# Kernel tuning notes

Hardware: AMD Instinct MI355X
Metric: run time of the kernel (lower is better)

Reference implementation:

```python
import jax, jax.numpy as jnp
import numpy as np

K_DIM = 768
HEADS = 8
HEAD_DIM = K_DIM // HEADS  # 96


def setup_inputs() -> dict:
    key = jax.random.key(0)
    ks = jax.random.split(key, 6)
    b, t = 4, 2048
    scale = 1.0 / np.sqrt(HEAD_DIM)
    return {
        "input_x": jax.random.normal(ks[0], (b, t, K_DIM), dtype=jnp.float32),
        "Wq": jax.random.normal(ks[1], (HEAD_DIM, HEAD_DIM), dtype=jnp.float32) * scale,
        "Wk": jax.random.normal(ks[2], (HEAD_DIM, HEAD_DIM), dtype=jnp.float32) * scale,
        "Wv": jax.random.normal(ks[3], (HEAD_DIM, HEAD_DIM), dtype=jnp.float32) * scale,
        "Wu": jax.random.normal(ks[4], (K_DIM, K_DIM), dtype=jnp.float32) * (1.0 / np.sqrt(K_DIM)),
        "bu": jax.random.normal(ks[5], (K_DIM,), dtype=jnp.float32) * 0.01,
    }


def reference(input_x, Wq, Wk, Wv, Wu, bu):
    b, t, k = input_x.shape
    h, d = HEADS, k // HEADS
    # split into heads: [b, t, h, d]; per-head projections share the same d x d weights
    x = input_x.reshape(b, t, h, d)
    inv4 = 1.0 / (k ** 0.25)
    q = jnp.einsum("bthd,od->btho", x, Wq) * inv4  # scaled queries
    kk = jnp.einsum("bthd,od->btho", x, Wk) * inv4  # scaled keys
    v = jnp.einsum("bthd,od->btho", x, Wv)
    # full attention matrix [b, h, t, t] (materialized, as in the original bmm impl)
    scores = jnp.einsum("bthd,bshd->bhts", q, kk)
    attn = jax.nn.softmax(scores, axis=-1)
    out = jnp.einsum("bhts,bshd->bthd", attn, v).reshape(b, t, k)
    return out @ Wu.T + bu
```

## Files before the change

kernel.cpp:

```cpp
#include <hip/hip_runtime.h>
#include <hip/hip_bf16.h>
#include <math.h>

#define TB 2048
#define NB 4
#define NH 8
#define HD 96
#define KD 768

typedef unsigned short u16;
typedef __attribute__((ext_vector_type(4))) u16 u16x4;
typedef __attribute__((ext_vector_type(8))) u16 u16x8;
typedef __attribute__((ext_vector_type(4))) float f32x4;
typedef __attribute__((ext_vector_type(16))) float f32x16;
typedef __attribute__((ext_vector_type(4))) unsigned u32x4;
typedef __attribute__((ext_vector_type(8))) __bf16 bf16x8;

__device__ __forceinline__ u16 f2bf(float f) {
    unsigned u = __builtin_bit_cast(unsigned, f);
    u += 0x7FFFu + ((u >> 16) & 1u);
    return (u16)(u >> 16);
}
__device__ __forceinline__ bf16x8 cast8(u16x8 u) { return __builtin_bit_cast(bf16x8, u); }
__device__ __forceinline__ unsigned pkbf(float a, float b) {
    unsigned w;
    asm("v_cvt_pk_bf16_f32 %0, %1, %2" : "=v"(w) : "v"(a), "v"(b));
    return w;
}

__global__ __launch_bounds__(256) void qkv_proj(
    const float* __restrict__ x, const float* __restrict__ Wq,
    const float* __restrict__ Wk, const float* __restrict__ Wv,
    u16* __restrict__ Q, u16* __restrict__ Kout, u16* __restrict__ VT, float inv4)
{
    __shared__ __align__(16) u16 Wl[3][96][104];
    const int tid = threadIdx.x;
    for (int idx = tid; idx < 3 * 9216; idx += 256) {
        int m = idx / 9216, rem = idx % 9216;
        const float* Wsrc = (m == 0) ? Wq : (m == 1) ? Wk : Wv;
        float scale = (m < 2) ? inv4 : 1.0f;
        int r = rem / 96, c = rem % 96;
        Wl[m][r][c] = f2bf(Wsrc[rem] * scale);
    }
    __syncthreads();

    const int w = tid >> 6, l = tid & 63;
    const int lc = l & 15, lk = l >> 4;
    const int bh = blockIdx.y, b = bh >> 3, h = bh & 7;
    const int t0 = blockIdx.x * 64 + w * 16;

    bf16x8 afrag[3];
    {
        const float* xp = x + ((long)((b * TB + t0 + lc) * NH + h)) * HD + 8 * lk;
#pragma unroll
        for (int c = 0; c < 3; ++c) {
            f32x4 f0 = *(const f32x4*)(xp + c * 32);
            f32x4 f1 = *(const f32x4*)(xp + c * 32 + 4);
            u16x8 u;
#pragma unroll
            for (int j = 0; j < 4; ++j) { u[j] = f2bf(f0[j]); u[4 + j] = f2bf(f1[j]); }
            afrag[c] = cast8(u);
        }
    }

    const f32x4 Z4 = {0.f, 0.f, 0.f, 0.f};
    u16* outs[2] = {Q, Kout};
#pragma unroll
    for (int m = 0; m < 2; ++m) {
        f32x4 acc[6];
#pragma unroll
        for (int nt = 0; nt < 6; ++nt) acc[nt] = Z4;
#pragma unroll
        for (int c = 0; c < 3; ++c) {
#pragma unroll
            for (int nt = 0; nt < 6; ++nt) {
                u16x8 bw = *(const u16x8*)&Wl[m][nt * 16 + lc][c * 32 + 8 * lk];
                acc[nt] = __builtin_amdgcn_mfma_f32_16x16x32_bf16(afrag[c], cast8(bw), acc[nt], 0, 0, 0);
            }
        }
#pragma unroll
        for (int reg = 0; reg < 4; ++reg) {
            int t = t0 + lk * 4 + reg;
            u16* op = outs[m] + ((long)bh * TB + t) * HD;
#pragma unroll
            for (int nt = 0; nt < 6; ++nt)
                op[nt * 16 + lc] = f2bf(acc[nt][reg]);
        }
    }
    {
        f32x4 acc[6];
#pragma unroll
        for (int nt = 0; nt < 6; ++nt) acc[nt] = Z4;
#pragma unroll
        for (int c = 0; c < 3; ++c) {
#pragma unroll
            for (int nt = 0; nt < 6; ++nt) {
                u16x8 aw = *(const u16x8*)&Wl[2][nt * 16 + lc][c * 32 + 8 * lk];
                acc[nt] = __builtin_amdgcn_mfma_f32_16x16x32_bf16(cast8(aw), afrag[c], acc[nt], 0, 0, 0);
            }
        }
#pragma unroll
        for (int nt = 0; nt < 6; ++nt)
#pragma unroll
            for (int reg = 0; reg < 4; ++reg) {
                int o = nt * 16 + lk * 4 + reg;
                VT[((long)bh * HD + o) * TB + t0 + lc] = f2bf(acc[nt][reg]);
            }
    }
}

#define KOFF 0
#define VOFF (64 * 104)
#define SLAB (64 * 104 + 96 * 72)

__global__ __launch_bounds__(256) void attn(
    const u16* __restrict__ Q, const u16* __restrict__ Kin, const u16* __restrict__ VT,
    u16* __restrict__ O)
{
    __shared__ __align__(16) u16 SM[2][SLAB];

    const int tid = threadIdx.x;
    const int w = tid >> 6, l = tid & 63;
    const int m32 = l & 31, hi = l >> 5;
    const int lid = (blockIdx.x & 7) * 64 + (blockIdx.x >> 3);
    const int qt = lid & 15, bh = lid >> 4;
    const int q0 = qt * 128 + w * 32;

    const u16* Qb = Q + (long)bh * TB * HD;
    const u16* Kb = Kin + (long)bh * TB * HD;
    const u16* Vb = VT + (long)bh * HD * TB;

    const u16* gbase[6]; int loff[6]; int mult[6];
#pragma unroll
    for (int ci = 0; ci < 6; ++ci) {
        int ch = tid + ci * 256;
        if (ch < 768) {
            int row = ch / 12, cc = (ch % 12) * 8;
            gbase[ci] = Kb + row * HD + cc;
            mult[ci] = HD;
            loff[ci] = KOFF + row * 104 + cc;
        } else {
            int c2 = ch - 768;
            int d = c2 >> 3, sc = (c2 & 7) * 8;
            gbase[ci] = Vb + (long)d * TB + sc;
            mult[ci] = 1;
            loff[ci] = VOFF + d * 72 + sc;
        }
    }

    bf16x8 qb[6];
#pragma unroll
    for (int kk = 0; kk < 6; ++kk)
        qb[kk] = cast8(*(const u16x8*)(Qb + (long)(q0 + m32) * HD + kk * 16 + 8 * hi));

    u16x8 r[6];
#pragma unroll
    for (int ci = 0; ci < 6; ++ci) r[ci] = *(const u16x8*)(gbase[ci]);
#pragma unroll
    for (int ci = 0; ci < 6; ++ci) *(u16x8*)(SM[0] + loff[ci]) = r[ci];
#pragma unroll
    for (int ci = 0; ci < 6; ++ci) r[ci] = *(const u16x8*)(gbase[ci] + (long)64 * mult[ci]);

    float m_st = -1e30f, l_st = 0.f;
    f32x16 accO[3];
#pragma unroll
    for (int dt = 0; dt < 3; ++dt)
#pragma unroll
        for (int rr = 0; rr < 16; ++rr) accO[dt][rr] = 0.f;

    for (int st = 0; st < TB / 64; ++st) {
        __syncthreads();
        if (st < TB / 64 - 1) {
            u16* dst = SM[(st + 1) & 1];
#pragma unroll
            for (int ci = 0; ci < 6; ++ci) *(u16x8*)(dst + loff[ci]) = r[ci];
            int s2 = (st + 2 < TB / 64 ? st + 2 : TB / 64 - 1) * 64;
#pragma unroll
            for (int ci = 0; ci < 6; ++ci) r[ci] = *(const u16x8*)(gbase[ci] + (long)s2 * mult[ci]);
        }
        const u16* KP = SM[st & 1] + KOFF;
        const u16* VP = SM[st & 1] + VOFF;

        f32x16 sa[2];
        __builtin_amdgcn_s_setprio(1);
#pragma unroll
        for (int st2 = 0; st2 < 2; ++st2) {
#pragma unroll
            for (int rr = 0; rr < 16; ++rr) sa[st2][rr] = 0.f;
#pragma unroll
            for (int kk = 0; kk < 6; ++kk) {
                u16x8 kf = *(const u16x8*)(KP + (st2 * 32 + m32) * 104 + kk * 16 + 8 * hi);
                sa[st2] = __builtin_amdgcn_mfma_f32_32x32x16_bf16(cast8(kf), qb[kk], sa[st2], 0, 0, 0);
            }
        }
        __builtin_amdgcn_s_setprio(0);

        float tm = sa[0][0];
#pragma unroll
        for (int st2 = 0; st2 < 2; ++st2)
#pragma unroll
            for (int rr = 0; rr < 16; ++rr) tm = fmaxf(tm, sa[st2][rr]);
        tm = fmaxf(tm, __shfl_xor(tm, 32));
        if (!__all(tm - m_st <= 8.0f)) {
            float mnew = fmaxf(m_st, tm);
            float alpha = __expf(m_st - mnew);
#pragma unroll
            for (int dt = 0; dt < 3; ++dt)
#pragma unroll
                for (int rr = 0; rr < 16; ++rr) accO[dt][rr] *= alpha;
            l_st *= alpha;
            m_st = mnew;
        }
        float sum = 0.f;
#pragma unroll
        for (int st2 = 0; st2 < 2; ++st2)
#pragma unroll
            for (int rr = 0; rr < 16; ++rr) {
                float pv = __expf(sa[st2][rr] - m_st);
                sa[st2][rr] = pv;
                sum += pv;
            }
        sum += __shfl_xor(sum, 32);
        l_st += sum;

#pragma unroll
        for (int st2 = 0; st2 < 2; ++st2) {
            unsigned A1 = pkbf(sa[st2][0], sa[st2][1]);
            unsigned A2 = pkbf(sa[st2][2], sa[st2][3]);
            unsigned B1 = pkbf(sa[st2][4], sa[st2][5]);
            unsigned B2 = pkbf(sa[st2][6], sa[st2][7]);
            unsigned A3 = pkbf(sa[st2][8], sa[st2][9]);
            unsigned A4 = pkbf(sa[st2][10], sa[st2][11]);
            unsigned B3 = pkbf(sa[st2][12], sa[st2][13]);
            unsigned B4 = pkbf(sa[st2][14], sa[st2][15]);
            unsigned xA1 = __shfl_xor((int)A1, 32), xA2 = __shfl_xor((int)A2, 32);
            unsigned xB1 = __shfl_xor((int)B1, 32), xB2 = __shfl_xor((int)B2, 32);
            unsigned xA3 = __shfl_xor((int)A3, 32), xA4 = __shfl_xor((int)A4, 32);
            unsigned xB3 = __shfl_xor((int)B3, 32), xB4 = __shfl_xor((int)B4, 32);
            u32x4 t0 = { hi ? xB1 : A1, hi ? xB2 : A2, hi ? B1 : xA1, hi ? B2 : xA2 };
            u32x4 t1 = { hi ? xB3 : A3, hi ? xB4 : A4, hi ? B3 : xA3, hi ? B4 : xA4 };
            bf16x8 pb0 = __builtin_bit_cast(bf16x8, t0);
            bf16x8 pb1 = __builtin_bit_cast(bf16x8, t1);
            __builtin_amdgcn_s_setprio(1);
#pragma unroll
            for (int dt = 0; dt < 3; ++dt) {
                u16x8 vfa = *(const u16x8*)(VP + (dt * 32 + m32) * 72 + st2 * 32 + 8 * hi);
                accO[dt] = __builtin_amdgcn_mfma_f32_32x32x16_bf16(cast8(vfa), pb0, accO[dt], 0, 0, 0);
            }
#pragma unroll
            for (int dt = 0; dt < 3; ++dt) {
                u16x8 vfb = *(const u16x8*)(VP + (dt * 32 + m32) * 72 + st2 * 32 + 16 + 8 * hi);
                accO[dt] = __builtin_amdgcn_mfma_f32_32x32x16_bf16(cast8(vfb), pb1, accO[dt], 0, 0, 0);
            }
            __builtin_amdgcn_s_setprio(0);
        }
    }

    const int b = bh >> 3, h = bh & 7;
    float linv = 1.0f / l_st;
    int t = q0 + m32;
    u16* op = O + ((long)(b * TB + t)) * KD + h * HD;
#pragma unroll
    for (int dt = 0; dt < 3; ++dt)
#pragma unroll
        for (int q4 = 0; q4 < 4; ++q4) {
            u16x4 v = { f2bf(accO[dt][q4 * 4 + 0] * linv), f2bf(accO[dt][q4 * 4 + 1] * linv),
                        f2bf(accO[dt][q4 * 4 + 2] * linv), f2bf(accO[dt][q4 * 4 + 3] * linv) };
            *(u16x4*)(op + dt * 32 + q4 * 8 + 4 * hi) = v;
        }
}

__global__ __launch_bounds__(256) void wu_conv(const float* __restrict__ Wu, u16* __restrict__ Wub) {
    int i = (blockIdx.x * 256 + threadIdx.x) * 4;
    f32x4 f = *(const f32x4*)(Wu + i);
    u16x4 o = { f2bf(f[0]), f2bf(f[1]), f2bf(f[2]), f2bf(f[3]) };
    *(u16x4*)(Wub + i) = o;
}

__global__ __launch_bounds__(256) void out_gemm(
    const u16* __restrict__ O, const u16* __restrict__ Wub,
    const float* __restrict__ bu, float* __restrict__ out)
{
    __shared__ __align__(16) u16 Al[2][128][68];
    __shared__ __align__(16) u16 Bl[2][128][68];
    const int tid = threadIdx.x;
    const int w = tid >> 6, l = tid & 63;
    const int m32 = l & 31, hi = l >> 5;
    const int wr = w >> 1, wc = w & 1;
    const int lid = (blockIdx.x & 7) * 48 + (blockIdx.x >> 3);
    const int nb = lid % 6, mb = lid / 6;
    const int m0 = mb * 128, n0 = nb * 128;

    const int crow = tid >> 3, ccol = (tid & 7) * 8;

    f32x16 acc[2][2];
#pragma unroll
    for (int i = 0; i < 2; ++i)
#pragma unroll
        for (int j = 0; j < 2; ++j)
#pragma unroll
            for (int rr = 0; rr < 16; ++rr) acc[i][j][rr] = 0.f;

    u16x8 ra[4], rb[4];
#pragma unroll
    for (int i = 0; i < 4; ++i) {
        ra[i] = *(const u16x8*)(O   + (long)(m0 + crow + i * 32) * KD + ccol);
        rb[i] = *(const u16x8*)(Wub + (long)(n0 + crow + i * 32) * KD + ccol);
    }
#pragma unroll
    for (int i = 0; i < 4; ++i) {
        *(u16x8*)&Al[0][crow + i * 32][ccol] = ra[i];
        *(u16x8*)&Bl[0][crow + i * 32][ccol] = rb[i];
    }
#pragma unroll
    for (int i = 0; i < 4; ++i) {
        ra[i] = *(const u16x8*)(O   + (long)(m0 + crow + i * 32) * KD + 64 + ccol);
        rb[i] = *(const u16x8*)(Wub + (long)(n0 + crow + i * 32) * KD + 64 + ccol);
    }

    for (int kt = 0; kt < KD / 64; ++kt) {
        __syncthreads();
        if (kt < KD / 64 - 1) {
            int p = (kt + 1) & 1;
#pragma unroll
            for (int i = 0; i < 4; ++i) {
                *(u16x8*)&Al[p][crow + i * 32][ccol] = ra[i];
                *(u16x8*)&Bl[p][crow + i * 32][ccol] = rb[i];
            }
            int cn = (kt + 2 < KD / 64 ? kt + 2 : KD / 64 - 1) * 64;
#pragma unroll
            for (int i = 0; i < 4; ++i) {
                ra[i] = *(const u16x8*)(O   + (long)(m0 + crow + i * 32) * KD + cn + ccol);
                rb[i] = *(const u16x8*)(Wub + (long)(n0 + crow + i * 32) * KD + cn + ccol);
            }
        }
        int p = kt & 1;
        __builtin_amdgcn_s_setprio(1);
#pragma unroll
        for (int k16 = 0; k16 < 4; ++k16) {
            bf16x8 afr[2], bfr[2];
#pragma unroll
            for (int rb2 = 0; rb2 < 2; ++rb2)
                afr[rb2] = cast8(*(const u16x8*)&Al[p][wr * 64 + rb2 * 32 + m32][k16 * 16 + 8 * hi]);
#pragma unroll
            for (int cb2 = 0; cb2 < 2; ++cb2)
                bfr[cb2] = cast8(*(const u16x8*)&Bl[p][wc * 64 + cb2 * 32 + m32][k16 * 16 + 8 * hi]);
#pragma unroll
            for (int rb2 = 0; rb2 < 2; ++rb2)
#pragma unroll
                for (int cb2 = 0; cb2 < 2; ++cb2)
                    acc[rb2][cb2] = __builtin_amdgcn_mfma_f32_32x32x16_bf16(afr[rb2], bfr[cb2], acc[rb2][cb2], 0, 0, 0);
        }
        __builtin_amdgcn_s_setprio(0);
    }

    const float bv0 = bu[n0 + wc * 64 + m32];
    const float bv1 = bu[n0 + wc * 64 + 32 + m32];
#pragma unroll
    for (int rb2 = 0; rb2 < 2; ++rb2)
#pragma unroll
        for (int cb2 = 0; cb2 < 2; ++cb2) {
            float bv = cb2 ? bv1 : bv0;
            int nn = n0 + wc * 64 + cb2 * 32 + m32;
#pragma unroll
            for (int reg = 0; reg < 16; ++reg) {
                int mm = m0 + wr * 64 + rb2 * 32 + (reg & 3) + 8 * (reg >> 2) + 4 * hi;
                out[(long)mm * KD + nn] = acc[rb2][cb2][reg] + bv;
            }
        }
}

extern "C" void kernel_launch(void* const* d_in, const int* in_sizes, int n_in,
                              void* d_out, int out_size, void* d_ws, size_t ws_size,
                              hipStream_t stream) {
    const float* x  = (const float*)d_in[0];
    const float* Wq = (const float*)d_in[1];
    const float* Wk = (const float*)d_in[2];
    const float* Wv = (const float*)d_in[3];
    const float* Wu = (const float*)d_in[4];
    const float* bu = (const float*)d_in[5];
    float* out = (float*)d_out;

    u16* ws = (u16*)d_ws;
    const size_t SZ = (size_t)NB * NH * TB * HD;
    u16* Q   = ws;
    u16* Kq  = ws + SZ;
    u16* VT  = ws + 2 * SZ;
    u16* O   = ws + 3 * SZ;
    u16* Wub = ws;

    const float inv4 = 1.0f / powf((float)KD, 0.25f);

    qkv_proj<<<dim3(TB / 64, NB * NH), dim3(256), 0, stream>>>(x, Wq, Wk, Wv, Q, Kq, VT, inv4);
    attn<<<dim3(TB / 128 * NB * NH), dim3(256), 0, stream>>>(Q, Kq, VT, O);
    wu_conv<<<dim3((KD * KD) / 1024), dim3(256), 0, stream>>>(Wu, Wub);
    out_gemm<<<dim3((NB * TB / 128) * (KD / 128)), dim3(256), 0, stream>>>(O, Wub, bu, out);
}
```

Baseline: 208.8 us.

## Double query rows per wave in attention and stage QKV stores through LDS

The attention kernel now gives each wave 64 query rows (two 32-row sub-tiles) instead of 32, so each K/V fragment read from LDS feeds two MFMAs. The KV tile shrinks to 32 keys and the grid is halved, which cuts K/V global and LDS traffic per query. In exchange it raises register pressure from the doubled accumulators and leaves only 256 blocks. The QKV projection also stages its outputs in shared memory so Q/K/VT are written with coalesced 16-byte stores instead of scattered 2-byte stores, at the cost of extra barriers.

```diff
diff --git a/kernel.cpp b/kernel.cpp
--- a/kernel.cpp
+++ b/kernel.cpp
@@ -34,6 +34,7 @@
     u16* __restrict__ Q, u16* __restrict__ Kout, u16* __restrict__ VT, float inv4)
 {
     __shared__ __align__(16) u16 Wl[3][96][104];
+    __shared__ __align__(16) u16 Rp[96 * 72];
     const int tid = threadIdx.x;
     for (int idx = tid; idx < 3 * 9216; idx += 256) {
         int m = idx / 9216, rem = idx % 9216;
@@ -47,11 +48,12 @@
     const int w = tid >> 6, l = tid & 63;
     const int lc = l & 15, lk = l >> 4;
     const int bh = blockIdx.y, b = bh >> 3, h = bh & 7;
-    const int t0 = blockIdx.x * 64 + w * 16;
+    const int t0 = blockIdx.x * 64;
+    const int tw = t0 + w * 16;
 
     bf16x8 afrag[3];
     {
-        const float* xp = x + ((long)((b * TB + t0 + lc) * NH + h)) * HD + 8 * lk;
+        const float* xp = x + ((long)((b * TB + tw + lc) * NH + h)) * HD + 8 * lk;
 #pragma unroll
         for (int c = 0; c < 3; ++c) {
             f32x4 f0 = *(const f32x4*)(xp + c * 32);
@@ -78,13 +80,18 @@
                 acc[nt] = __builtin_amdgcn_mfma_f32_16x16x32_bf16(afrag[c], cast8(bw), acc[nt], 0, 0, 0);
             }
         }
-#pragma unroll
-        for (int reg = 0; reg < 4; ++reg) {
-            int t = t0 + lk * 4 + reg;
-            u16* op = outs[m] + ((long)bh * TB + t) * HD;
-#pragma unroll
-            for (int nt = 0; nt < 6; ++nt)
-                op[nt * 16 + lc] = f2bf(acc[nt][reg]);
+        __syncthreads();
+#pragma unroll
+        for (int nt = 0; nt < 6; ++nt)
+#pragma unroll
+            for (int reg = 0; reg < 4; ++reg)
+                Rp[(w * 16 + lk * 4 + reg) * 104 + nt * 16 + lc] = f2bf(acc[nt][reg]);
+        __syncthreads();
+#pragma unroll
+        for (int ci = 0; ci < 3; ++ci) {
+            int ch = tid + ci * 256;
+            int row = ch / 12, cc = (ch % 12) * 8;
+            *(u16x8*)(outs[m] + ((long)bh * TB + t0 + row) * HD + cc) = *(const u16x8*)&Rp[row * 104 + cc];
         }
     }
     {
@@ -99,175 +106,199 @@
                 acc[nt] = __builtin_amdgcn_mfma_f32_16x16x32_bf16(cast8(aw), afrag[c], acc[nt], 0, 0, 0);
             }
         }
+        __syncthreads();
 #pragma unroll
         for (int nt = 0; nt < 6; ++nt)
 #pragma unroll
             for (int reg = 0; reg < 4; ++reg) {
                 int o = nt * 16 + lk * 4 + reg;
-                VT[((long)bh * HD + o) * TB + t0 + lc] = f2bf(acc[nt][reg]);
-            }
-    }
-}
-
-#define KOFF 0
-#define VOFF (64 * 104)
-#define SLAB (64 * 104 + 96 * 72)
+                Rp[o * 72 + w * 16 + lc] = f2bf(acc[nt][reg]);
+            }
+        __syncthreads();
+#pragma unroll
+        for (int ci = 0; ci < 3; ++ci) {
+            int ch = tid + ci * 256;
+            int row = ch >> 3, tc = (ch & 7) * 8;
+            *(u16x8*)(VT + ((long)bh * HD + row) * TB + t0 + tc) = *(const u16x8*)&Rp[row * 72 + tc];
+        }
+    }
+}
+
+#define KVB 32
+#define VOFF2 (KVB * 104)
+#define SLAB2 (KVB * 104 + 96 * 40)
 
 __global__ __launch_bounds__(256) void attn(
     const u16* __restrict__ Q, const u16* __restrict__ Kin, const u16* __restrict__ VT,
     u16* __restrict__ O)
 {
-    __shared__ __align__(16) u16 SM[2][SLAB];
+    __shared__ __align__(16) u16 SM[2][SLAB2];
 
     const int tid = threadIdx.x;
     const int w = tid >> 6, l = tid & 63;
     const int m32 = l & 31, hi = l >> 5;
-    const int lid = (blockIdx.x & 7) * 64 + (blockIdx.x >> 3);
-    const int qt = lid & 15, bh = lid >> 4;
-    const int q0 = qt * 128 + w * 32;
+    const int lid = (blockIdx.x & 7) * 32 + (blockIdx.x >> 3);
+    const int qt = lid & 7, bh = lid >> 3;
+    const int q0 = qt * 256 + w * 64;
 
     const u16* Qb = Q + (long)bh * TB * HD;
     const u16* Kb = Kin + (long)bh * TB * HD;
     const u16* Vb = VT + (long)bh * HD * TB;
 
-    const u16* gbase[6]; int loff[6]; int mult[6];
-#pragma unroll
-    for (int ci = 0; ci < 6; ++ci) {
+    const u16* gbase[3]; int loff[3]; int mult[3];
+#pragma unroll
+    for (int ci = 0; ci < 3; ++ci) {
         int ch = tid + ci * 256;
-        if (ch < 768) {
+        if (ch < 384) {
             int row = ch / 12, cc = (ch % 12) * 8;
             gbase[ci] = Kb + row * HD + cc;
             mult[ci] = HD;
-            loff[ci] = KOFF + row * 104 + cc;
+            loff[ci] = row * 104 + cc;
         } else {
-            int c2 = ch - 768;
-            int d = c2 >> 3, sc = (c2 & 7) * 8;
+            int c2 = ch - 384;
+            int d = c2 >> 2, sc = (c2 & 3) * 8;
             gbase[ci] = Vb + (long)d * TB + sc;
             mult[ci] = 1;
-            loff[ci] = VOFF + d * 72 + sc;
-        }
-    }
-
-    bf16x8 qb[6];
-#pragma unroll
-    for (int kk = 0; kk < 6; ++kk)
-        qb[kk] = cast8(*(const u16x8*)(Qb + (long)(q0 + m32) * HD + kk * 16 + 8 * hi));
-
-    u16x8 r[6];
-#pragma unroll
-    for (int ci = 0; ci < 6; ++ci) r[ci] = *(const u16x8*)(gbase[ci]);
-#pragma unroll
-    for (int ci = 0; ci < 6; ++ci) *(u16x8*)(SM[0] + loff[ci]) = r[ci];
-#pragma unroll
-    for (int ci = 0; ci < 6; ++ci) r[ci] = *(const u16x8*)(gbase[ci] + (long)64 * mult[ci]);
-
-    float m_st = -1e30f, l_st = 0.f;
-    f32x16 accO[3];
+            loff[ci] = VOFF2 + d * 40 + sc;
+        }
+    }
+
+    bf16x8 qb[2][6];
+#pragma unroll
+    for (int qs = 0; qs < 2; ++qs)
+#pragma unroll
+        for (int kk = 0; kk < 6; ++kk)
+            qb[qs][kk] = cast8(*(const u16x8*)(Qb + (long)(q0 + qs * 32 + m32) * HD + kk * 16 + 8 * hi));
+
+    u16x8 r[3];
+#pragma unroll
+    for (int ci = 0; ci < 3; ++ci) r[ci] = *(const u16x8*)(gbase[ci]);
+#pragma unroll
+    for (int ci = 0; ci < 3; ++ci) *(u16x8*)(SM[0] + loff[ci]) = r[ci];
+#pragma unroll
+    for (int ci = 0; ci < 3; ++ci) r[ci] = *(const u16x8*)(gbase[ci] + (long)KVB * mult[ci]);
+
+    float m_st[2] = {-1e30f, -1e30f}, l_st[2] = {0.f, 0.f};
+    f32x16 accO[3][2];
 #pragma unroll
     for (int dt = 0; dt < 3; ++dt)
 #pragma unroll
-        for (int rr = 0; rr < 16; ++rr) accO[dt][rr] = 0.f;
-
-    for (int st = 0; st < TB / 64; ++st) {
-        __syncthreads();
-        if (st < TB / 64 - 1) {
+        for (int qs = 0; qs < 2; ++qs)
+#pragma unroll
+            for (int rr = 0; rr < 16; ++rr) accO[dt][qs][rr] = 0.f;
+
+    const int NST = TB / KVB;
+    for (int st = 0; st < NST; ++st) {
+        __syncthreads();
+        if (st < NST - 1) {
             u16* dst = SM[(st + 1) & 1];
 #pragma unroll
-            for (int ci = 0; ci < 6; ++ci) *(u16x8*)(dst + loff[ci]) = r[ci];
-            int s2 = (st + 2 < TB / 64 ? st + 2 : TB / 64 - 1) * 64;
-#pragma unroll
-            for (int ci = 0; ci < 6; ++ci) r[ci] = *(const u16x8*)(gbase[ci] + (long)s2 * mult[ci]);
-        }
-        const u16* KP = SM[st & 1] + KOFF;
-        const u16* VP = SM[st & 1] + VOFF;
+            for (int ci = 0; ci < 3; ++ci) *(u16x8*)(dst + loff[ci]) = r[ci];
+            int s2 = (st + 2 < NST ? st + 2 : NST - 1) * KVB;
+#pragma unroll
+            for (int ci = 0; ci < 3; ++ci) r[ci] = *(const u16x8*)(gbase[ci] + (long)s2 * mult[ci]);
+        }
+        const u16* KP = SM[st & 1];
+        const u16* VP = SM[st & 1] + VOFF2;
 
         f32x16 sa[2];
+#pragma unroll
+        for (int qs = 0; qs < 2; ++qs)
+#pragma unroll
+            for (int rr = 0; rr < 16; ++rr) sa[qs][rr] = 0.f;
         __builtin_amdgcn_s_setprio(1);
 #pragma unroll
-        for (int st2 = 0; st2 < 2; ++st2) {
-#pragma unroll
-            for (int rr = 0; rr < 16; ++rr) sa[st2][rr] = 0.f;
-#pragma unroll
-            for (int kk = 0; kk < 6; ++kk) {
-                u16x8 kf = *(const u16x8*)(KP + (st2 * 32 + m32) * 104 + kk * 16 + 8 * hi);
-                sa[st2] = __builtin_amdgcn_mfma_f32_32x32x16_bf16(cast8(kf), qb[kk], sa[st2], 0, 0, 0);
-            }
+        for (int kk = 0; kk < 6; ++kk) {
+            u16x8 kf = *(const u16x8*)(KP + m32 * 104 + kk * 16 + 8 * hi);
+            sa[0] = __builtin_amdgcn_mfma_f32_32x32x16_bf16(cast8(kf), qb[0][kk], sa[0], 0, 0, 0);
+            sa[1] = __builtin_amdgcn_mfma_f32_32x32x16_bf16(cast8(kf), qb[1][kk], sa[1], 0, 0, 0);
         }
         __builtin_amdgcn_s_setprio(0);
 
-        float tm = sa[0][0];
-#pragma unroll
-        for (int st2 = 0; st2 < 2; ++st2)
-#pragma unroll
-            for (int rr = 0; rr < 16; ++rr) tm = fmaxf(tm, sa[st2][rr]);
-        tm = fmaxf(tm, __shfl_xor(tm, 32));
-        if (!__all(tm - m_st <= 8.0f)) {
-            float mnew = fmaxf(m_st, tm);
-            float alpha = __expf(m_st - mnew);
-#pragma unroll
-            for (int dt = 0; dt < 3; ++dt)
-#pragma unroll
-                for (int rr = 0; rr < 16; ++rr) accO[dt][rr] *= alpha;
-            l_st *= alpha;
-            m_st = mnew;
-        }
-        float sum = 0.f;
-#pragma unroll
-        for (int st2 = 0; st2 < 2; ++st2)
+        float tm[2];
+#pragma unroll
+        for (int qs = 0; qs < 2; ++qs) {
+            float t2 = sa[qs][0];
+#pragma unroll
+            for (int rr = 1; rr < 16; ++rr) t2 = fmaxf(t2, sa[qs][rr]);
+            t2 = fmaxf(t2, __shfl_xor(t2, 32));
+            tm[qs] = t2;
+        }
+        if (!__all(tm[0] - m_st[0] <= 8.0f && tm[1] - m_st[1] <= 8.0f)) {
+#pragma unroll
+            for (int qs = 0; qs < 2; ++qs) {
+                float mnew = fmaxf(m_st[qs], tm[qs]);
+                float alpha = __expf(m_st[qs] - mnew);
+#pragma unroll
+                for (int dt = 0; dt < 3; ++dt)
+#pragma unroll
+                    for (int rr = 0; rr < 16; ++rr) accO[dt][qs][rr] *= alpha;
+                l_st[qs] *= alpha;
+                m_st[qs] = mnew;
+            }
+        }
+#pragma unroll
+        for (int qs = 0; qs < 2; ++qs) {
+            float sum = 0.f;
 #pragma unroll
             for (int rr = 0; rr < 16; ++rr) {
-                float pv = __expf(sa[st2][rr] - m_st);
-                sa[st2][rr] = pv;
+                float pv = __expf(sa[qs][rr] - m_st[qs]);
+                sa[qs][rr] = pv;
                 sum += pv;
             }
-        sum += __shfl_xor(sum, 32);
-        l_st += sum;
-
-#pragma unroll
-        for (int st2 = 0; st2 < 2; ++st2) {
-            unsigned A1 = pkbf(sa[st2][0], sa[st2][1]);
-            unsigned A2 = pkbf(sa[st2][2], sa[st2][3]);
-            unsigned B1 = pkbf(sa[st2][4], sa[st2][5]);
-            unsigned B2 = pkbf(sa[st2][6], sa[st2][7]);
-            unsigned A3 = pkbf(sa[st2][8], sa[st2][9]);
-            unsigned A4 = pkbf(sa[st2][10], sa[st2][11]);
-            unsigned B3 = pkbf(sa[st2][12], sa[st2][13]);
-            unsigned B4 = pkbf(sa[st2][14], sa[st2][15]);
+            sum += __shfl_xor(sum, 32);
+            l_st[qs] += sum;
+        }
+
+        bf16x8 pb0[2], pb1[2];
+#pragma unroll
+        for (int qs = 0; qs < 2; ++qs) {
+            unsigned A1 = pkbf(sa[qs][0], sa[qs][1]);
+            unsigned A2 = pkbf(sa[qs][2], sa[qs][3]);
+            unsigned B1 = pkbf(sa[qs][4], sa[qs][5]);
+            unsigned B2 = pkbf(sa[qs][6], sa[qs][7]);
+            unsigned A3 = pkbf(sa[qs][8], sa[qs][9]);
+            unsigned A4 = pkbf(sa[qs][10], sa[qs][11]);
+            unsigned B3 = pkbf(sa[qs][12], sa[qs][13]);
+            unsigned B4 = pkbf(sa[qs][14], sa[qs][15]);
             unsigned xA1 = __shfl_xor((int)A1, 32), xA2 = __shfl_xor((int)A2, 32);
             unsigned xB1 = __shfl_xor((int)B1, 32), xB2 = __shfl_xor((int)B2, 32);
             unsigned xA3 = __shfl_xor((int)A3, 32), xA4 = __shfl_xor((int)A4, 32);
             unsigned xB3 = __shfl_xor((int)B3, 32), xB4 = __shfl_xor((int)B4, 32);
-            u32x4 t0 = { hi ? xB1 : A1, hi ? xB2 : A2, hi ? B1 : xA1, hi ? B2 : xA2 };
-            u32x4 t1 = { hi ? xB3 : A3, hi ? xB4 : A4, hi ? B3 : xA3, hi ? B4 : xA4 };
-            bf16x8 pb0 = __builtin_bit_cast(bf16x8, t0);
-            bf16x8 pb1 = __builtin_bit_cast(bf16x8, t1);
-            __builtin_amdgcn_s_setprio(1);
-#pragma unroll
-            for (int dt = 0; dt < 3; ++dt) {
-                u16x8 vfa = *(const u16x8*)(VP + (dt * 32 + m32) * 72 + st2 * 32 + 8 * hi);
-                accO[dt] = __builtin_amdgcn_mfma_f32_32x32x16_bf16(cast8(vfa), pb0, accO[dt], 0, 0, 0);
-            }
-#pragma unroll
-            for (int dt = 0; dt < 3; ++dt) {
-                u16x8 vfb = *(const u16x8*)(VP + (dt * 32 + m32) * 72 + st2 * 32 + 16 + 8 * hi);
-                accO[dt] = __builtin_amdgcn_mfma_f32_32x32x16_bf16(cast8(vfb), pb1, accO[dt], 0, 0, 0);
-            }
-            __builtin_amdgcn_s_setprio(0);
-        }
+            u32x4 t0v = { hi ? xB1 : A1, hi ? xB2 : A2, hi ? B1 : xA1, hi ? B2 : xA2 };
+            u32x4 t1v = { hi ? xB3 : A3, hi ? xB4 : A4, hi ? B3 : xA3, hi ? B4 : xA4 };
+            pb0[qs] = __builtin_bit_cast(bf16x8, t0v);
+            pb1[qs] = __builtin_bit_cast(bf16x8, t1v);
+        }
+
+        __builtin_amdgcn_s_setprio(1);
+#pragma unroll
+        for (int dt = 0; dt < 3; ++dt) {
+            u16x8 vf0 = *(const u16x8*)(VP + (dt * 32 + m32) * 40 + 8 * hi);
+            accO[dt][0] = __builtin_amdgcn_mfma_f32_32x32x16_bf16(cast8(vf0), pb0[0], accO[dt][0], 0, 0, 0);
+            accO[dt][1] = __builtin_amdgcn_mfma_f32_32x32x16_bf16(cast8(vf0), pb0[1], accO[dt][1], 0, 0, 0);
+            u16x8 vf1 = *(const u16x8*)(VP + (dt * 32 + m32) * 40 + 16 + 8 * hi);
+            accO[dt][0] = __builtin_amdgcn_mfma_f32_32x32x16_bf16(cast8(vf1), pb1[0], accO[dt][0], 0, 0, 0);
+            accO[dt][1] = __builtin_amdgcn_mfma_f32_32x32x16_bf16(cast8(vf1), pb1[1], accO[dt][1], 0, 0, 0);
+        }
+        __builtin_amdgcn_s_setprio(0);
     }
 
     const int b = bh >> 3, h = bh & 7;
-    float linv = 1.0f / l_st;
-    int t = q0 + m32;
-    u16* op = O + ((long)(b * TB + t)) * KD + h * HD;
-#pragma unroll
-    for (int dt = 0; dt < 3; ++dt)
-#pragma unroll
-        for (int q4 = 0; q4 < 4; ++q4) {
-            u16x4 v = { f2bf(accO[dt][q4 * 4 + 0] * linv), f2bf(accO[dt][q4 * 4 + 1] * linv),
-                        f2bf(accO[dt][q4 * 4 + 2] * linv), f2bf(accO[dt][q4 * 4 + 3] * linv) };
-            *(u16x4*)(op + dt * 32 + q4 * 8 + 4 * hi) = v;
-        }
+#pragma unroll
+    for (int qs = 0; qs < 2; ++qs) {
+        float linv = 1.0f / l_st[qs];
+        int t = q0 + qs * 32 + m32;
+        u16* op = O + ((long)(b * TB + t)) * KD + h * HD;
+#pragma unroll
+        for (int dt = 0; dt < 3; ++dt)
+#pragma unroll
+            for (int g = 0; g < 4; ++g) {
+                u16x4 v = { f2bf(accO[dt][qs][g * 4 + 0] * linv), f2bf(accO[dt][qs][g * 4 + 1] * linv),
+                            f2bf(accO[dt][qs][g * 4 + 2] * linv), f2bf(accO[dt][qs][g * 4 + 3] * linv) };
+                *(u16x4*)(op + dt * 32 + g * 8 + 4 * hi) = v;
+            }
+    }
 }
 
 __global__ __launch_bounds__(256) void wu_conv(const float* __restrict__ Wu, u16* __restrict__ Wub) {
@@ -392,7 +423,7 @@
     const float inv4 = 1.0f / powf((float)KD, 0.25f);
 
     qkv_proj<<<dim3(TB / 64, NB * NH), dim3(256), 0, stream>>>(x, Wq, Wk, Wv, Q, Kq, VT, inv4);
-    attn<<<dim3(TB / 128 * NB * NH), dim3(256), 0, stream>>>(Q, Kq, VT, O);
+    attn<<<dim3(TB / 256 * NB * NH), dim3(256), 0, stream>>>(Q, Kq, VT, O);
     wu_conv<<<dim3((KD * KD) / 1024), dim3(256), 0, stream>>>(Wu, Wub);
     out_gemm<<<dim3((NB * TB / 128) * (KD / 128)), dim3(256), 0, stream>>>(O, Wub, bu, out);
 }
```

Measured after the change: 232.2 us. 1.11x slower.
